# Optimization experiments

Hardware: AMD Instinct MI355X
Metric: run time of the kernel (lower is better)

The kernel has to match this reference:

```python
import jax, jax.numpy as jnp
import numpy as np

B, N, F_IN, F_OUT, E = 8, 20000, 128, 128, 320000
ALPHA = 0.2  # LeakyReLU negative slope


def _xavier_normal(key, shape, gain=1.414):
    fan_in, fan_out = shape[0], shape[1]
    std = gain * np.sqrt(2.0 / (fan_in + fan_out))
    return jax.random.normal(key, shape, dtype=jnp.float32) * std


def setup_inputs() -> dict:
    key = jax.random.key(0)
    k1, k2, k3, k4, k5 = jax.random.split(key, 5)
    x = jax.random.normal(k1, (B, N, F_IN), dtype=jnp.float32)
    W = _xavier_normal(k2, (F_IN, F_OUT))
    a = _xavier_normal(k3, (2 * F_OUT, 1))
    # Edge list (src, dst). First N src are arange so every row has >=1 edge
    # (avoids div-by-zero in rowsum, matching a graph with no isolated sources).
    src_extra = jax.random.randint(k4, (E - N,), 0, N, dtype=jnp.int32)
    src = jnp.concatenate([jnp.arange(N, dtype=jnp.int32), src_extra])
    dst = jax.random.randint(k5, (E,), 0, N, dtype=jnp.int32)
    edge = jnp.stack([src, dst], axis=0)  # [2, E]
    return {"x": x, "W": W, "a": a, "edge": edge}


def reference(x, W, a, edge):
    # x: [B, N, F_in], W: [F_in, F_out], a: [2*F_out, 1], edge: [2, E]
    Fo = W.shape[1]
    n = x.shape[1]
    src, dst = edge[0], edge[1]
    h = jnp.einsum('bnf,fo->bno', x, W)  # [B, N, Fo]
    # cat(h[src], h[dst]) @ a  ==  (h @ a1)[src] + (h @ a2)[dst]
    a1, a2 = a[:Fo, 0], a[Fo:, 0]
    s = (h @ a1)[:, src] + (h @ a2)[:, dst]  # [B, E]
    score = jnp.where(s > 0, s, ALPHA * s)  # LeakyReLU
    e = jnp.exp(-score)  # [B, E]
    # spmm: h_prime[src] += e * h[dst]; rowsum[src] += e  (per batch)
    msg = e[..., None] * h[:, dst, :]  # [B, E, Fo]
    seg = jax.vmap(lambda m: jax.ops.segment_sum(m, src, num_segments=n))(msg)  # [B,N,Fo]
    rowsum = jax.vmap(lambda v: jax.ops.segment_sum(v, src, num_segments=n))(e)  # [B,N]
    h_prime = seg / rowsum[..., None]
    return jax.nn.elu(h_prime)  # concat=True -> ELU
```

## Files before the change

### kernel.cpp

```cpp
#include <hip/hip_runtime.h>

#define NB 8
#define NN 20000
#define FI 128
#define FO 128
#define NE 320000
#define ROWS (NB * NN)
#define LRALPHA 0.2f

typedef short bf16x8 __attribute__((ext_vector_type(8)));
typedef float f32x4 __attribute__((ext_vector_type(4)));

static __device__ __forceinline__ float b2f(unsigned short u) {
  return __uint_as_float(((unsigned int)u) << 16);
}
static __device__ __forceinline__ unsigned short f2b(float f) {
  unsigned int u = __float_as_uint(f);
  return (unsigned short)((u + 0x7FFFu + ((u >> 16) & 1u)) >> 16);
}

#define LDW 136

__global__ __launch_bounds__(256) void gemm_kernel(
    const float* __restrict__ x, const float* __restrict__ W,
    const float* __restrict__ a,
    unsigned short* __restrict__ hb,
    float* __restrict__ g1, float* __restrict__ g2) {
  __shared__ __align__(16) unsigned short Wt[128 * LDW];
  __shared__ __align__(16) unsigned short Xs[64 * LDW];
  const int tid = threadIdx.x;

  for (int i = 0; i < 64; ++i) {
    int idx = tid + i * 256;
    int k = idx >> 7, n = idx & 127;
    Wt[n * LDW + k] = f2b(W[idx]);
  }
  const size_t row0 = (size_t)blockIdx.x * 64;
  const float4* xv = (const float4*)(x + row0 * 128);
  for (int i = 0; i < 8; ++i) {
    int c = tid + i * 256;
    float4 v = xv[c];
    int r = c >> 5;
    int k = (c & 31) * 4;
    ushort4 o;
    o.x = f2b(v.x); o.y = f2b(v.y); o.z = f2b(v.z); o.w = f2b(v.w);
    *(ushort4*)&Xs[r * LDW + k] = o;
  }
  __syncthreads();

  const int wv = tid >> 6;
  const int lane = tid & 63;
  const int m = lane & 15;
  const int quad = lane >> 4;
  f32x4 acc[8] = {};
#pragma unroll
  for (int k0 = 0; k0 < 128; k0 += 32) {
    bf16x8 af = *(const bf16x8*)&Xs[(wv * 16 + m) * LDW + k0 + quad * 8];
#pragma unroll
    for (int c = 0; c < 8; ++c) {
      bf16x8 bf = *(const bf16x8*)&Wt[(c * 16 + m) * LDW + k0 + quad * 8];
      acc[c] = __builtin_amdgcn_mfma_f32_16x16x32_bf16(af, bf, acc[c], 0, 0, 0);
    }
  }
  unsigned short* hp = hb + (row0 + (size_t)wv * 16) * 128;
#pragma unroll
  for (int c = 0; c < 8; ++c)
#pragma unroll
    for (int r = 0; r < 4; ++r)
      hp[(quad * 4 + r) * 128 + c * 16 + m] = f2b(acc[c][r]);

  float a1v[8], a2v[8];
#pragma unroll
  for (int c = 0; c < 8; ++c) {
    a1v[c] = a[c * 16 + m];
    a2v[c] = a[128 + c * 16 + m];
  }
  float p1[4] = {}, p2[4] = {};
#pragma unroll
  for (int c = 0; c < 8; ++c)
#pragma unroll
    for (int r = 0; r < 4; ++r) {
      p1[r] = fmaf(acc[c][r], a1v[c], p1[r]);
      p2[r] = fmaf(acc[c][r], a2v[c], p2[r]);
    }
#pragma unroll
  for (int off = 1; off < 16; off <<= 1)
#pragma unroll
    for (int r = 0; r < 4; ++r) {
      p1[r] += __shfl_xor(p1[r], off, 64);
      p2[r] += __shfl_xor(p2[r], off, 64);
    }
  if (m == 0) {
    size_t rbase = row0 + wv * 16 + quad * 4;
#pragma unroll
    for (int r = 0; r < 4; ++r) {
      g1[rbase + r] = p1[r];
      g2[rbase + r] = p2[r];
    }
  }
}

__global__ __launch_bounds__(256) void hist_kernel(const int* __restrict__ src,
                                                   int* __restrict__ counts) {
  int e = blockIdx.x * 256 + threadIdx.x;
  if (e < NE) atomicAdd(&counts[src[e]], 1);
}

__global__ __launch_bounds__(1024) void scan_kernel(
    const int* __restrict__ counts, int* __restrict__ offsets,
    int* __restrict__ cursor) {
  __shared__ int sc[NN];
  __shared__ int sums[1024];
  const int t = threadIdx.x;
  for (int idx = t; idx < NN; idx += 1024) sc[idx] = counts[idx];
  __syncthreads();
  int local[20];
  int base = t * 20;
  int s = 0;
#pragma unroll
  for (int c = 0; c < 20; ++c) {
    int idx = base + c;
    int v = (idx < NN) ? sc[idx] : 0;
    local[c] = s;
    s += v;
  }
  sums[t] = s;
  __syncthreads();
  for (int off = 1; off < 1024; off <<= 1) {
    int u = 0;
    if (t >= off) u = sums[t - off];
    __syncthreads();
    sums[t] += u;
    __syncthreads();
  }
  int prefix = sums[t] - s;
#pragma unroll
  for (int c = 0; c < 20; ++c) {
    int idx = base + c;
    if (idx < NN) {
      int o = prefix + local[c];
      offsets[idx] = o;
      cursor[idx] = o;
    }
  }
  if (t == 0) offsets[NN] = NE;
}

__global__ __launch_bounds__(256) void scatter_kernel(
    const int* __restrict__ src, int* __restrict__ cursor,
    int* __restrict__ elist) {
  int e = blockIdx.x * 256 + threadIdx.x;
  if (e < NE) {
    int s = src[e];
    int pos = atomicAdd(&cursor[s], 1);
    elist[pos] = e;
  }
}

__global__ __launch_bounds__(64) void gather_kernel(
    const unsigned short* __restrict__ hb, const float* __restrict__ g1,
    const float* __restrict__ g2, const int* __restrict__ dst,
    const int* __restrict__ offsets, const int* __restrict__ elist,
    float* __restrict__ out) {
  const int i = blockIdx.x;
  const int b = blockIdx.y;
  const int lane = threadIdx.x;
  const int beg = offsets[i];
  const int deg = offsets[i + 1] - beg;
  const float g1i = g1[(size_t)b * NN + i];
  const float* g2b = g2 + (size_t)b * NN;
  const unsigned short* hbb = hb + (size_t)b * NN * 128;

  float accx = 0.f, accy = 0.f, rs = 0.f;
  for (int c0 = 0; c0 < deg; c0 += 64) {
    const int cnt = min(64, deg - c0);
    int myd = 0;
    float w = 0.f;
    if (lane < cnt) {
      int e = elist[beg + c0 + lane];
      myd = dst[e];
      float s = g1i + g2b[myd];
      float sc = fmaxf(s, LRALPHA * s);
      w = __expf(-sc);
    }
    rs += w;
    const int cr = (cnt + 7) & ~7;
    for (int e = 0; e < cr; e += 8) {
      ushort2 hv[8];
      float we[8];
#pragma unroll
      for (int j = 0; j < 8; ++j) {
        int d = __shfl(myd, e + j, 64);
        we[j] = __shfl(w, e + j, 64);
        hv[j] = *(const ushort2*)&hbb[(size_t)d * 128 + 2 * lane];
      }
#pragma unroll
      for (int j = 0; j < 8; ++j) {
        accx = fmaf(we[j], b2f(hv[j].x), accx);
        accy = fmaf(we[j], b2f(hv[j].y), accy);
      }
    }
  }
#pragma unroll
  for (int off = 32; off >= 1; off >>= 1) rs += __shfl_xor(rs, off, 64);
  float inv = 1.f / rs;
  float ox = accx * inv, oy = accy * inv;
  ox = ox > 0.f ? ox : expm1f(ox);
  oy = oy > 0.f ? oy : expm1f(oy);
  float2* op = (float2*)(out + ((size_t)b * NN + i) * 128);
  op[lane] = make_float2(ox, oy);
}

extern "C" void kernel_launch(void* const* d_in, const int* in_sizes, int n_in,
                              void* d_out, int out_size, void* d_ws, size_t ws_size,
                              hipStream_t stream) {
  const float* x = (const float*)d_in[0];
  const float* W = (const float*)d_in[1];
  const float* a = (const float*)d_in[2];
  const int* edge = (const int*)d_in[3];
  const int* src = edge;
  const int* dst = edge + NE;
  float* out = (float*)d_out;

  char* p = (char*)d_ws;
  unsigned short* hb = (unsigned short*)p;  p += (size_t)ROWS * 128 * 2;
  float* g1 = (float*)p;                    p += (size_t)ROWS * 4;
  float* g2 = (float*)p;                    p += (size_t)ROWS * 4;
  int* counts = (int*)p;                    p += (size_t)NN * 4;
  int* offsets = (int*)p;                   p += (size_t)(NN + 1) * 4;
  int* cursor = (int*)p;                    p += (size_t)NN * 4;
  int* elist = (int*)p;                     p += (size_t)NE * 4;

  hipMemsetAsync(counts, 0, NN * sizeof(int), stream);
  gemm_kernel<<<ROWS / 64, 256, 0, stream>>>(x, W, a, hb, g1, g2);
  hist_kernel<<<(NE + 255) / 256, 256, 0, stream>>>(src, counts);
  scan_kernel<<<1, 1024, 0, stream>>>(counts, offsets, cursor);
  scatter_kernel<<<(NE + 255) / 256, 256, 0, stream>>>(src, cursor, elist);
  dim3 ggrid(NN, NB);
  gather_kernel<<<ggrid, 64, 0, stream>>>(hb, g1, g2, dst, offsets, elist, out);
}
```

Before: 301.3 us.

## Pre-convert W once, load GEMM operands from global, store dst directly in CSR

W is converted to bf16 and transposed once by a new small kernel. It was previously converted into LDS by every GEMM block. The GEMM now loads x fragments straight into registers and reads W fragments from global/L2, which removes the LDS staging and the barrier. The scatter step writes destination indices into the CSR array directly, so the gather kernel no longer does a dependent elist->dst indirection. The costs are one extra launch and uncoalesced strided x loads.

Measured after the change: 330.2 us. 9.6% more time.

```diff
diff --git a/kernel.cpp b/kernel.cpp
--- a/kernel.cpp
+++ b/kernel.cpp
@@ -19,50 +19,51 @@
   return (unsigned short)((u + 0x7FFFu + ((u >> 16) & 1u)) >> 16);
 }
 
-#define LDW 136
+__global__ __launch_bounds__(256) void wt_kernel(const float* __restrict__ W,
+                                                 unsigned short* __restrict__ Wb) {
+  int idx = blockIdx.x * 256 + threadIdx.x;
+  int k = idx >> 7, o = idx & 127;
+  Wb[o * 128 + k] = f2b(W[idx]);
+}
 
 __global__ __launch_bounds__(256) void gemm_kernel(
-    const float* __restrict__ x, const float* __restrict__ W,
+    const float* __restrict__ x, const unsigned short* __restrict__ Wb,
     const float* __restrict__ a,
     unsigned short* __restrict__ hb,
     float* __restrict__ g1, float* __restrict__ g2) {
-  __shared__ __align__(16) unsigned short Wt[128 * LDW];
-  __shared__ __align__(16) unsigned short Xs[64 * LDW];
   const int tid = threadIdx.x;
-
-  for (int i = 0; i < 64; ++i) {
-    int idx = tid + i * 256;
-    int k = idx >> 7, n = idx & 127;
-    Wt[n * LDW + k] = f2b(W[idx]);
-  }
-  const size_t row0 = (size_t)blockIdx.x * 64;
-  const float4* xv = (const float4*)(x + row0 * 128);
-  for (int i = 0; i < 8; ++i) {
-    int c = tid + i * 256;
-    float4 v = xv[c];
-    int r = c >> 5;
-    int k = (c & 31) * 4;
-    ushort4 o;
-    o.x = f2b(v.x); o.y = f2b(v.y); o.z = f2b(v.z); o.w = f2b(v.w);
-    *(ushort4*)&Xs[r * LDW + k] = o;
-  }
-  __syncthreads();
-
   const int wv = tid >> 6;
   const int lane = tid & 63;
   const int m = lane & 15;
   const int quad = lane >> 4;
+  const size_t row0 = (size_t)blockIdx.x * 64 + wv * 16;
+
+  const float* xr = x + (row0 + m) * 128;
+  bf16x8 afr[4];
+#pragma unroll
+  for (int k0 = 0; k0 < 4; ++k0) {
+    const float4* xp = (const float4*)(xr + k0 * 32 + quad * 8);
+    float4 v0 = xp[0];
+    float4 v1 = xp[1];
+    union { bf16x8 v; unsigned short u[8]; } af;
+    af.u[0] = f2b(v0.x); af.u[1] = f2b(v0.y);
+    af.u[2] = f2b(v0.z); af.u[3] = f2b(v0.w);
+    af.u[4] = f2b(v1.x); af.u[5] = f2b(v1.y);
+    af.u[6] = f2b(v1.z); af.u[7] = f2b(v1.w);
+    afr[k0] = af.v;
+  }
+
   f32x4 acc[8] = {};
 #pragma unroll
-  for (int k0 = 0; k0 < 128; k0 += 32) {
-    bf16x8 af = *(const bf16x8*)&Xs[(wv * 16 + m) * LDW + k0 + quad * 8];
+  for (int k0 = 0; k0 < 4; ++k0) {
 #pragma unroll
     for (int c = 0; c < 8; ++c) {
-      bf16x8 bf = *(const bf16x8*)&Wt[(c * 16 + m) * LDW + k0 + quad * 8];
-      acc[c] = __builtin_amdgcn_mfma_f32_16x16x32_bf16(af, bf, acc[c], 0, 0, 0);
-    }
-  }
-  unsigned short* hp = hb + (row0 + (size_t)wv * 16) * 128;
+      bf16x8 bf = *(const bf16x8*)&Wb[(c * 16 + m) * 128 + k0 * 32 + quad * 8];
+      acc[c] = __builtin_amdgcn_mfma_f32_16x16x32_bf16(afr[k0], bf, acc[c], 0, 0, 0);
+    }
+  }
+
+  unsigned short* hp = hb + row0 * 128;
 #pragma unroll
   for (int c = 0; c < 8; ++c)
 #pragma unroll
@@ -91,7 +92,7 @@
       p2[r] += __shfl_xor(p2[r], off, 64);
     }
   if (m == 0) {
-    size_t rbase = row0 + wv * 16 + quad * 4;
+    size_t rbase = row0 + quad * 4;
 #pragma unroll
     for (int r = 0; r < 4; ++r) {
       g1[rbase + r] = p1[r];
@@ -147,21 +148,21 @@
 }
 
 __global__ __launch_bounds__(256) void scatter_kernel(
-    const int* __restrict__ src, int* __restrict__ cursor,
-    int* __restrict__ elist) {
+    const int* __restrict__ src, const int* __restrict__ dst,
+    int* __restrict__ cursor, int* __restrict__ csr_dst) {
   int e = blockIdx.x * 256 + threadIdx.x;
   if (e < NE) {
     int s = src[e];
+    int d = dst[e];
     int pos = atomicAdd(&cursor[s], 1);
-    elist[pos] = e;
+    csr_dst[pos] = d;
   }
 }
 
 __global__ __launch_bounds__(64) void gather_kernel(
     const unsigned short* __restrict__ hb, const float* __restrict__ g1,
-    const float* __restrict__ g2, const int* __restrict__ dst,
-    const int* __restrict__ offsets, const int* __restrict__ elist,
-    float* __restrict__ out) {
+    const float* __restrict__ g2, const int* __restrict__ offsets,
+    const int* __restrict__ csr_dst, float* __restrict__ out) {
   const int i = blockIdx.x;
   const int b = blockIdx.y;
   const int lane = threadIdx.x;
@@ -177,8 +178,7 @@
     int myd = 0;
     float w = 0.f;
     if (lane < cnt) {
-      int e = elist[beg + c0 + lane];
-      myd = dst[e];
+      myd = csr_dst[beg + c0 + lane];
       float s = g1i + g2b[myd];
       float sc = fmaxf(s, LRALPHA * s);
       w = __expf(-sc);
@@ -229,13 +229,15 @@
   int* counts = (int*)p;                    p += (size_t)NN * 4;
   int* offsets = (int*)p;                   p += (size_t)(NN + 1) * 4;
   int* cursor = (int*)p;                    p += (size_t)NN * 4;
-  int* elist = (int*)p;                     p += (size_t)NE * 4;
+  int* csr_dst = (int*)p;                   p += (size_t)NE * 4;
+  unsigned short* Wb = (unsigned short*)p;  p += (size_t)FI * FO * 2;
 
   hipMemsetAsync(counts, 0, NN * sizeof(int), stream);
-  gemm_kernel<<<ROWS / 64, 256, 0, stream>>>(x, W, a, hb, g1, g2);
+  wt_kernel<<<64, 256, 0, stream>>>(W, Wb);
+  gemm_kernel<<<ROWS / 64, 256, 0, stream>>>(x, Wb, a, hb, g1, g2);
   hist_kernel<<<(NE + 255) / 256, 256, 0, stream>>>(src, counts);
   scan_kernel<<<1, 1024, 0, stream>>>(counts, offsets, cursor);
-  scatter_kernel<<<(NE + 255) / 256, 256, 0, stream>>>(src, cursor, elist);
+  scatter_kernel<<<(NE + 255) / 256, 256, 0, stream>>>(src, dst, cursor, csr_dst);
   dim3 ggrid(NN, NB);
-  gather_kernel<<<ggrid, 64, 0, stream>>>(hb, g1, g2, dst, offsets, elist, out);
-}
+  gather_kernel<<<ggrid, 64, 0, stream>>>(hb, g1, g2, offsets, csr_dst, out);
+}
```
